# Kernel tuning notes

Hardware: AMD Instinct MI355X
Metric: run time of the kernel (lower is better)

Reference implementation:

```python
import jax, jax.numpy as jnp
import numpy as np

NX, NY = 100, 100
FLOW_EXP = 1.25          # 5/4
K_SHEET = 0.01           # sheet_conductivity
K_CHAN = 0.1             # channel_conductivity
CAVITY_SPACING = 2.0
ICE_RHO, WATER_RHO, LATENT = 917.0, 1000.0, 3.34e5
DISS = (1.0 / ICE_RHO - 1.0 / WATER_RHO) / LATENT  # dissipation_coeff


def _build_grid(nx, ny):
    """Raster grid: degree-4 adjacency (E,W,N,S) with -1 padding, aligned link ids."""
    N = nx * ny
    xg, yg = np.meshgrid(np.arange(nx), np.arange(ny))
    x, y = xg.ravel(), yg.ravel()
    nid = y * nx + x
    nh = (nx - 1) * ny  # number of horizontal links
    adj = -np.ones((N, 4), np.int64)
    lnk = -np.ones((N, 4), np.int64)
    e = x < nx - 1
    adj[e, 0] = nid[e] + 1;  lnk[e, 0] = y[e] * (nx - 1) + x[e]
    w = x > 0
    adj[w, 1] = nid[w] - 1;  lnk[w, 1] = y[w] * (nx - 1) + x[w] - 1
    no = y < ny - 1
    adj[no, 2] = nid[no] + nx;  lnk[no, 2] = nh + y[no] * nx + x[no]
    so = y > 0
    adj[so, 3] = nid[so] - nx;  lnk[so, 3] = nh + (y[so] - 1) * nx + x[so]
    ids = np.arange(N).reshape(ny, nx)
    tail = np.concatenate([ids[:, :-1].ravel(), ids[:-1, :].ravel()])
    head = np.concatenate([ids[:, 1:].ravel(), ids[1:, :].ravel()])
    boundary = (x == 0) | (x == nx - 1) | (y == 0) | (y == ny - 1)
    inout = np.where(boundary, 1, -1).astype(np.int32)
    return (adj.astype(np.int32), lnk.astype(np.int32),
            head.astype(np.int32), tail.astype(np.int32), inout)


def setup_inputs() -> dict:
    key = jax.random.key(0)
    k = jax.random.split(key, 5)
    adj, lnk, head, tail, inout = _build_grid(NX, NY)
    N = NX * NY
    L = head.size
    pot = jax.random.normal(k[0], (N,), jnp.float32) * 1e4 + 1e6
    channel_size = jax.random.uniform(k[1], (L,), jnp.float32, 0.1, 2.0)
    sheet = jax.random.uniform(k[2], (N,), jnp.float32, 0.01, 0.5)
    face_len = jax.random.uniform(k[3], (L,), jnp.float32, 50.0, 150.0)
    link_len = jax.random.uniform(k[4], (L,), jnp.float32, 50.0, 150.0)
    return dict(previous_potential=pot, channel_size=channel_size,
                sheet_thickness=sheet, length_of_face=face_len,
                length_of_link=link_len,
                adjacent_nodes=jnp.asarray(adj), links_at_node=jnp.asarray(lnk),
                face_at_link=jnp.arange(L, dtype=jnp.int32),
                link_head=jnp.asarray(head), link_tail=jnp.asarray(tail),
                inflow_outflow=jnp.asarray(inout))


def reference(previous_potential, channel_size, sheet_thickness,
              length_of_face, length_of_link, adjacent_nodes, links_at_node,
              face_at_link, link_head, link_tail, inflow_outflow):
    N = previous_potential.shape[0]
    # --- link fields ---
    grad = (previous_potential[link_head] - previous_potential[link_tail]) / length_of_link  # [L]
    chan_q = -K_CHAN * channel_size ** FLOW_EXP * grad                                        # [L]
    st_link = 0.5 * (sheet_thickness[link_head] + sheet_thickness[link_tail])
    sheet_q = -K_SHEET * st_link ** FLOW_EXP * jnp.abs(grad) ** (-0.5) * grad                 # [L]
    # --- per (node, neighbor-slot) terms, [N,4] ---
    mask = adjacent_nodes != -1
    j = jnp.where(mask, adjacent_nodes, 0)
    lid = jnp.where(mask, links_at_node, 0)
    fl = length_of_face[face_at_link[lid]]
    ll = length_of_link[lid]
    i_idx = jnp.arange(N)[:, None]
    # NOTE: source indexes channel_size (a link field) by node id; reproduced faithfully.
    cs = 0.5 * (channel_size[i_idx] + channel_size[j])
    st = 0.5 * (sheet_thickness[i_idx] + sheet_thickness[j])
    g = grad[lid]
    sheet_flux = -K_SHEET * st ** FLOW_EXP * jnp.abs(g) ** (-0.5) * fl / ll
    chan_flux = -K_CHAN * cs ** FLOW_EXP * fl / ll
    ch_diss = jnp.abs(DISS * chan_q[lid] * fl)
    sh_diss = jnp.abs(DISS * sheet_q[lid] * CAVITY_SPACING * fl)
    term = jnp.where(mask, sheet_flux + chan_flux + ch_diss + sh_diss, 0.0)  # [N,4]
    # --- assemble dense operator ---
    M = jnp.zeros((N, N), previous_potential.dtype)
    rows = jnp.broadcast_to(i_idx, term.shape)
    M = M.at[rows, j].add(-term)                       # off-diagonal scatter
    M = M.at[jnp.arange(N), jnp.arange(N)].add(term.sum(axis=1))  # diagonal
    bnd = inflow_outflow == 1
    M = jnp.where(bnd[:, None], jnp.eye(N, dtype=M.dtype), M)     # Dirichlet rows
    return M
```

## Files before the change

### kernel.cpp

```cpp
#include <hip/hip_runtime.h>
#include <math.h>

#define K_SHEET   0.01f
#define K_CHAN    0.1f
#define CAV_SPACE 2.0f
#define FLOW_EXP  1.25f

__device__ __constant__ float c_diss = (float)((1.0 / 917.0 - 1.0 / 1000.0) / 3.34e5);

__global__ void sgds_patch_kernel(const float* __restrict__ pot,
                                  const float* __restrict__ chan,
                                  const float* __restrict__ sheet,
                                  const float* __restrict__ face_len,
                                  const float* __restrict__ link_len,
                                  const int*   __restrict__ adj,
                                  const int*   __restrict__ lnk,
                                  const int*   __restrict__ face_at_link,
                                  const int*   __restrict__ head,
                                  const int*   __restrict__ tail,
                                  const int*   __restrict__ inout,
                                  float*       __restrict__ M,
                                  int N)
{
    int i = blockIdx.x * blockDim.x + threadIdx.x;
    if (i >= N) return;

    float* row = M + (size_t)i * (size_t)N;

    if (inout[i] == 1) {
        row[i] = 1.0f;
        return;
    }

    float diag = 0.0f;

    #pragma unroll
    for (int s = 0; s < 4; ++s) {
        int j = adj[i * 4 + s];
        if (j < 0) continue;
        int lid = lnk[i * 4 + s];

        int   h  = head[lid];
        int   t  = tail[lid];
        float ll = link_len[lid];
        float g  = (pot[h] - pot[t]) / ll;

        float cq  = -K_CHAN * powf(chan[lid], FLOW_EXP) * g;
        float stl = 0.5f * (sheet[h] + sheet[t]);
        float ginv_sqrt = 1.0f / sqrtf(fabsf(g));
        float sq  = -K_SHEET * powf(stl, FLOW_EXP) * ginv_sqrt * g;

        float fl = face_len[face_at_link[lid]];
        float cs = 0.5f * (chan[i] + chan[j]);
        float st = 0.5f * (sheet[i] + sheet[j]);

        float sheet_flux = -K_SHEET * powf(st, FLOW_EXP) * ginv_sqrt * fl / ll;
        float chan_flux  = -K_CHAN  * powf(cs, FLOW_EXP) * fl / ll;
        float ch_diss    = fabsf(c_diss * cq * fl);
        float sh_diss    = fabsf(c_diss * sq * CAV_SPACE * fl);

        float term = sheet_flux + chan_flux + ch_diss + sh_diss;

        row[j] = -term;
        diag  += term;
    }

    row[i] = diag;
}

extern "C" void kernel_launch(void* const* d_in, const int* in_sizes, int n_in,
                              void* d_out, int out_size, void* d_ws, size_t ws_size,
                              hipStream_t stream) {
    const float* pot      = (const float*)d_in[0];
    const float* chan     = (const float*)d_in[1];
    const float* sheet    = (const float*)d_in[2];
    const float* face_len = (const float*)d_in[3];
    const float* link_len = (const float*)d_in[4];
    const int*   adj      = (const int*)d_in[5];
    const int*   lnk      = (const int*)d_in[6];
    const int*   fal      = (const int*)d_in[7];
    const int*   head     = (const int*)d_in[8];
    const int*   tail     = (const int*)d_in[9];
    const int*   inout    = (const int*)d_in[10];

    float* M = (float*)d_out;
    int N = in_sizes[0];

    hipMemsetAsync(d_out, 0, (size_t)out_size * sizeof(float), stream);

    int block = 256;
    int grid  = (N + block - 1) / block;
    sgds_patch_kernel<<<grid, block, 0, stream>>>(pot, chan, sheet, face_len, link_len,
                                                  adj, lnk, fal, head, tail, inout, M, N);
}
```

Measured before the change: 416.4 us.

## Fuse matrix zero-fill with row assembly in one row-per-block kernel

Replaces the separate memset plus sparse scatter kernel with a single kernel where each block owns one matrix row. Thread 0 computes the up to five nonzeros into shared memory, and all threads then write the full row with float4 stores, inserting the nonzeros where they fall. This removes the extra launch and the second pass over the 400 MB output, at the cost of a block-level sync and a per-chunk scan of the nonzero list. The float4 path assumes each row starts 16-byte aligned, which holds since N is a multiple of 4.

```diff
diff --git a/kernel.cpp b/kernel.cpp
--- a/kernel.cpp
+++ b/kernel.cpp
@@ -8,64 +8,86 @@
 
 __device__ __constant__ float c_diss = (float)((1.0 / 917.0 - 1.0 / 1000.0) / 3.34e5);
 
-__global__ void sgds_patch_kernel(const float* __restrict__ pot,
-                                  const float* __restrict__ chan,
-                                  const float* __restrict__ sheet,
-                                  const float* __restrict__ face_len,
-                                  const float* __restrict__ link_len,
-                                  const int*   __restrict__ adj,
-                                  const int*   __restrict__ lnk,
-                                  const int*   __restrict__ face_at_link,
-                                  const int*   __restrict__ head,
-                                  const int*   __restrict__ tail,
-                                  const int*   __restrict__ inout,
-                                  float*       __restrict__ M,
-                                  int N)
+__global__ __launch_bounds__(256) void sgds_row_kernel(
+        const float* __restrict__ pot,
+        const float* __restrict__ chan,
+        const float* __restrict__ sheet,
+        const float* __restrict__ face_len,
+        const float* __restrict__ link_len,
+        const int*   __restrict__ adj,
+        const int*   __restrict__ lnk,
+        const int*   __restrict__ face_at_link,
+        const int*   __restrict__ head,
+        const int*   __restrict__ tail,
+        const int*   __restrict__ inout,
+        float*       __restrict__ M,
+        int N)
 {
-    int i = blockIdx.x * blockDim.x + threadIdx.x;
-    if (i >= N) return;
+    __shared__ int   s_col[8];
+    __shared__ float s_val[8];
+    __shared__ int   s_cnt;
 
+    const int i = blockIdx.x;
     float* row = M + (size_t)i * (size_t)N;
 
-    if (inout[i] == 1) {
-        row[i] = 1.0f;
-        return;
+    if (threadIdx.x == 0) {
+        int cnt = 0;
+        if (inout[i] == 1) {
+            s_col[0] = i; s_val[0] = 1.0f; cnt = 1;
+        } else {
+            float diag = 0.0f;
+            #pragma unroll
+            for (int s = 0; s < 4; ++s) {
+                int j = adj[i * 4 + s];
+                if (j < 0) continue;
+                int lid = lnk[i * 4 + s];
+
+                int   h  = head[lid];
+                int   t  = tail[lid];
+                float ll = link_len[lid];
+                float g  = (pot[h] - pot[t]) / ll;
+
+                float cq  = -K_CHAN * powf(chan[lid], FLOW_EXP) * g;
+                float stl = 0.5f * (sheet[h] + sheet[t]);
+                float gis = 1.0f / sqrtf(fabsf(g));
+                float sq  = -K_SHEET * powf(stl, FLOW_EXP) * gis * g;
+
+                float fl = face_len[face_at_link[lid]];
+                float cs = 0.5f * (chan[i] + chan[j]);
+                float st = 0.5f * (sheet[i] + sheet[j]);
+
+                float sheet_flux = -K_SHEET * powf(st, FLOW_EXP) * gis * fl / ll;
+                float chan_flux  = -K_CHAN  * powf(cs, FLOW_EXP) * fl / ll;
+                float ch_diss    = fabsf(c_diss * cq * fl);
+                float sh_diss    = fabsf(c_diss * sq * CAV_SPACE * fl);
+
+                float term = sheet_flux + chan_flux + ch_diss + sh_diss;
+                s_col[cnt] = j; s_val[cnt] = -term; ++cnt;
+                diag += term;
+            }
+            s_col[cnt] = i; s_val[cnt] = diag; ++cnt;
+        }
+        s_cnt = cnt;
     }
+    __syncthreads();
 
-    float diag = 0.0f;
-
-    #pragma unroll
-    for (int s = 0; s < 4; ++s) {
-        int j = adj[i * 4 + s];
-        if (j < 0) continue;
-        int lid = lnk[i * 4 + s];
-
-        int   h  = head[lid];
-        int   t  = tail[lid];
-        float ll = link_len[lid];
-        float g  = (pot[h] - pot[t]) / ll;
-
-        float cq  = -K_CHAN * powf(chan[lid], FLOW_EXP) * g;
-        float stl = 0.5f * (sheet[h] + sheet[t]);
-        float ginv_sqrt = 1.0f / sqrtf(fabsf(g));
-        float sq  = -K_SHEET * powf(stl, FLOW_EXP) * ginv_sqrt * g;
-
-        float fl = face_len[face_at_link[lid]];
-        float cs = 0.5f * (chan[i] + chan[j]);
-        float st = 0.5f * (sheet[i] + sheet[j]);
-
-        float sheet_flux = -K_SHEET * powf(st, FLOW_EXP) * ginv_sqrt * fl / ll;
-        float chan_flux  = -K_CHAN  * powf(cs, FLOW_EXP) * fl / ll;
-        float ch_diss    = fabsf(c_diss * cq * fl);
-        float sh_diss    = fabsf(c_diss * sq * CAV_SPACE * fl);
-
-        float term = sheet_flux + chan_flux + ch_diss + sh_diss;
-
-        row[j] = -term;
-        diag  += term;
+    const int cnt = s_cnt;
+    const int chunks = N >> 2;
+    float4* row4 = reinterpret_cast<float4*>(row);
+    for (int c = threadIdx.x; c < chunks; c += blockDim.x) {
+        float4 v = make_float4(0.0f, 0.0f, 0.0f, 0.0f);
+        const int base = c << 2;
+        for (int k = 0; k < cnt; ++k) {
+            int d = s_col[k] - base;
+            if ((unsigned)d < 4u) (&v.x)[d] = s_val[k];
+        }
+        row4[c] = v;
     }
-
-    row[i] = diag;
+    for (int c = (chunks << 2) + (int)threadIdx.x; c < N; c += blockDim.x) {
+        float v = 0.0f;
+        for (int k = 0; k < cnt; ++k) if (s_col[k] == c) v = s_val[k];
+        row[c] = v;
+    }
 }
 
 extern "C" void kernel_launch(void* const* d_in, const int* in_sizes, int n_in,
@@ -86,10 +108,6 @@
     float* M = (float*)d_out;
     int N = in_sizes[0];
 
-    hipMemsetAsync(d_out, 0, (size_t)out_size * sizeof(float), stream);
-
-    int block = 256;
-    int grid  = (N + block - 1) / block;
-    sgds_patch_kernel<<<grid, block, 0, stream>>>(pot, chan, sheet, face_len, link_len,
-                                                  adj, lnk, fal, head, tail, inout, M, N);
+    sgds_row_kernel<<<N, 256, 0, stream>>>(pot, chan, sheet, face_len, link_len,
+                                           adj, lnk, fal, head, tail, inout, M, N);
 }
```

Result: slower. 470.5 us (+13.0%).

## Fuse zero-fill and stencil writes into one vectorized flat kernel

Applied to the files above, without the earlier changes.

Drops the separate memset plus scatter kernel. A single grid-stride kernel now writes every float4 chunk of the dense matrix once, with nontemporal stores. Chunks near the five stencil diagonals recompute that row's coefficients and merge them into the vector. The diagonal test hardcodes the grid width of 100, so it only holds for this grid shape and assumes N is divisible by 4.

```diff
diff --git a/kernel.cpp b/kernel.cpp
--- a/kernel.cpp
+++ b/kernel.cpp
@@ -5,67 +5,96 @@
 #define K_CHAN    0.1f
 #define CAV_SPACE 2.0f
 #define FLOW_EXP  1.25f
+#define NXG       100
 
 __device__ __constant__ float c_diss = (float)((1.0 / 917.0 - 1.0 / 1000.0) / 3.34e5);
 
-__global__ void sgds_patch_kernel(const float* __restrict__ pot,
-                                  const float* __restrict__ chan,
-                                  const float* __restrict__ sheet,
-                                  const float* __restrict__ face_len,
-                                  const float* __restrict__ link_len,
-                                  const int*   __restrict__ adj,
-                                  const int*   __restrict__ lnk,
-                                  const int*   __restrict__ face_at_link,
-                                  const int*   __restrict__ head,
-                                  const int*   __restrict__ tail,
-                                  const int*   __restrict__ inout,
-                                  float*       __restrict__ M,
-                                  int N)
+typedef float f4 __attribute__((ext_vector_type(4)));
+
+__global__ __launch_bounds__(256) void sgds_fused_flat(
+        const float* __restrict__ pot,
+        const float* __restrict__ chan,
+        const float* __restrict__ sheet,
+        const float* __restrict__ face_len,
+        const float* __restrict__ link_len,
+        const int*   __restrict__ adj,
+        const int*   __restrict__ lnk,
+        const int*   __restrict__ face_at_link,
+        const int*   __restrict__ head,
+        const int*   __restrict__ tail,
+        const int*   __restrict__ inout,
+        float*       __restrict__ M,
+        int N)
 {
-    int i = blockIdx.x * blockDim.x + threadIdx.x;
-    if (i >= N) return;
+    const int tid      = blockIdx.x * blockDim.x + threadIdx.x;
+    const int nthreads = gridDim.x * blockDim.x;
+    const int nchunks  = (N / 4) * N;
 
-    float* row = M + (size_t)i * (size_t)N;
+    f4* __restrict__ M4 = reinterpret_cast<f4*>(M);
 
-    if (inout[i] == 1) {
-        row[i] = 1.0f;
-        return;
+    for (int c = tid; c < nchunks; c += nthreads) {
+        const int b  = c << 2;
+        const int r  = (int)((unsigned)b / (unsigned)N);
+        const int cb = b - r * N;
+
+        const bool hit = ((unsigned)((r - NXG) - cb) < 4u) |
+                         ((unsigned)((r - 1  ) - cb) < 4u) |
+                         ((unsigned)((r      ) - cb) < 4u) |
+                         ((unsigned)((r + 1  ) - cb) < 4u) |
+                         ((unsigned)((r + NXG) - cb) < 4u);
+
+        f4 v = (f4)(0.0f);
+
+        if (__builtin_expect(hit, 0)) {
+            #define MERGE(col, val)                          \
+                do {                                          \
+                    int _c = (col); float _v = (val);         \
+                    v.x = (_c == cb    ) ? _v : v.x;          \
+                    v.y = (_c == cb + 1) ? _v : v.y;          \
+                    v.z = (_c == cb + 2) ? _v : v.z;          \
+                    v.w = (_c == cb + 3) ? _v : v.w;          \
+                } while (0)
+
+            if (inout[r] == 1) {
+                MERGE(r, 1.0f);
+            } else {
+                float diag = 0.0f;
+                #pragma unroll
+                for (int s = 0; s < 4; ++s) {
+                    int j = adj[r * 4 + s];
+                    if (j < 0) continue;
+                    int lid = lnk[r * 4 + s];
+
+                    int   h  = head[lid];
+                    int   t  = tail[lid];
+                    float ll = link_len[lid];
+                    float g  = (pot[h] - pot[t]) / ll;
+
+                    float cq  = -K_CHAN * powf(chan[lid], FLOW_EXP) * g;
+                    float stl = 0.5f * (sheet[h] + sheet[t]);
+                    float gis = 1.0f / sqrtf(fabsf(g));
+                    float sq  = -K_SHEET * powf(stl, FLOW_EXP) * gis * g;
+
+                    float fl = face_len[face_at_link[lid]];
+                    float cs = 0.5f * (chan[r] + chan[j]);
+                    float st = 0.5f * (sheet[r] + sheet[j]);
+
+                    float sheet_flux = -K_SHEET * powf(st, FLOW_EXP) * gis * fl / ll;
+                    float chan_flux  = -K_CHAN  * powf(cs, FLOW_EXP) * fl / ll;
+                    float ch_diss    = fabsf(c_diss * cq * fl);
+                    float sh_diss    = fabsf(c_diss * sq * CAV_SPACE * fl);
+
+                    float term = sheet_flux + chan_flux + ch_diss + sh_diss;
+                    MERGE(j, -term);
+                    diag += term;
+                }
+                MERGE(r, diag);
+            }
+            #undef MERGE
+        }
+
+        __builtin_nontemporal_store(v, M4 + c);
     }
-
-    float diag = 0.0f;
-
-    #pragma unroll
-    for (int s = 0; s < 4; ++s) {
-        int j = adj[i * 4 + s];
-        if (j < 0) continue;
-        int lid = lnk[i * 4 + s];
-
-        int   h  = head[lid];
-        int   t  = tail[lid];
-        float ll = link_len[lid];
-        float g  = (pot[h] - pot[t]) / ll;
-
-        float cq  = -K_CHAN * powf(chan[lid], FLOW_EXP) * g;
-        float stl = 0.5f * (sheet[h] + sheet[t]);
-        float ginv_sqrt = 1.0f / sqrtf(fabsf(g));
-        float sq  = -K_SHEET * powf(stl, FLOW_EXP) * ginv_sqrt * g;
-
-        float fl = face_len[face_at_link[lid]];
-        float cs = 0.5f * (chan[i] + chan[j]);
-        float st = 0.5f * (sheet[i] + sheet[j]);
-
-        float sheet_flux = -K_SHEET * powf(st, FLOW_EXP) * ginv_sqrt * fl / ll;
-        float chan_flux  = -K_CHAN  * powf(cs, FLOW_EXP) * fl / ll;
-        float ch_diss    = fabsf(c_diss * cq * fl);
-        float sh_diss    = fabsf(c_diss * sq * CAV_SPACE * fl);
-
-        float term = sheet_flux + chan_flux + ch_diss + sh_diss;
-
-        row[j] = -term;
-        diag  += term;
-    }
-
-    row[i] = diag;
 }
 
 extern "C" void kernel_launch(void* const* d_in, const int* in_sizes, int n_in,
@@ -86,10 +115,6 @@
     float* M = (float*)d_out;
     int N = in_sizes[0];
 
-    hipMemsetAsync(d_out, 0, (size_t)out_size * sizeof(float), stream);
-
-    int block = 256;
-    int grid  = (N + block - 1) / block;
-    sgds_patch_kernel<<<grid, block, 0, stream>>>(pot, chan, sheet, face_len, link_len,
-                                                  adj, lnk, fal, head, tail, inout, M, N);
+    sgds_fused_flat<<<2048, 256, 0, stream>>>(pot, chan, sheet, face_len, link_len,
+                                              adj, lnk, fal, head, tail, inout, M, N);
 }
```

Result: slower. 473.0 us (+13.6%).
